# Kernel optimization log

Hardware: AMD Instinct MI355X
Metric: run time of the kernel (lower is better)

Reference implementation:

```python
import jax, jax.numpy as jnp
import numpy as np

N_HEAD = 16
N_KV = 4
HEAD_DIM = 128
ROPE_BASE = 10000.0
YARN_ORIG = 2048
YARN_TARGET = 8192
YARN_ALPHA = 1.0
YARN_BETA = 1.0
SOFTCAP = 50.0


def _yarn_freqs(seq_len, start=0):
    # inv_freq with YaRN scaling: stretch by (target/orig)**alpha, magnitude 1/beta
    inv_freq = 1.0 / (ROPE_BASE ** (jnp.arange(0, HEAD_DIM, 2, dtype=jnp.float32) / HEAD_DIM))
    scale = (YARN_TARGET / YARN_ORIG) ** YARN_ALPHA
    inv_freq = inv_freq / scale * (1.0 / max(YARN_BETA, 1e-6))
    pos = jnp.arange(start, start + seq_len, dtype=jnp.float32)
    return pos[:, None] * inv_freq[None, :]  # [T, D/2]


def _apply_rope(x, freqs):
    # x: [B, H, T, D], interleaved even/odd rotation
    x_even = x[..., ::2]
    x_odd = x[..., 1::2]
    cos = jnp.cos(freqs)[None, None]  # [1,1,T,D/2]
    sin = jnp.sin(freqs)[None, None]
    y_even = x_even * cos - x_odd * sin
    y_odd = x_odd * cos + x_even * sin
    y = jnp.stack([y_even, y_odd], axis=-1).reshape(x.shape)
    return y


def setup_inputs() -> dict:
    key = jax.random.key(0)
    k1, k2, k3 = jax.random.split(key, 3)
    B, T, C = 2, 2048, 2048
    qkv_dim = (N_HEAD + 2 * N_KV) * HEAD_DIM  # 3072
    x = jax.random.normal(k1, (B, T, C), dtype=jnp.float32)
    w_qkv = jax.random.normal(k2, (C, qkv_dim), dtype=jnp.float32) * (1.0 / np.sqrt(C))
    w_o = jax.random.normal(k3, (C, C), dtype=jnp.float32) * (1.0 / np.sqrt(C))
    return {"x": x, "w_qkv": w_qkv, "w_o": w_o}


def reference(x, w_qkv, w_o):
    B, T, C = x.shape
    qkv = x @ w_qkv  # [B, T, (H+2*Hkv)*D]
    q_dim = N_HEAD * HEAD_DIM
    kv_dim = N_KV * HEAD_DIM
    q = qkv[..., :q_dim].reshape(B, T, N_HEAD, HEAD_DIM).transpose(0, 2, 1, 3)
    k = qkv[..., q_dim:q_dim + kv_dim].reshape(B, T, N_KV, HEAD_DIM).transpose(0, 2, 1, 3)
    v = qkv[..., q_dim + kv_dim:].reshape(B, T, N_KV, HEAD_DIM).transpose(0, 2, 1, 3)

    freqs = _yarn_freqs(T)
    q = _apply_rope(q, freqs)
    k = _apply_rope(k, freqs)

    # GQA: expand kv heads to query heads
    rep = N_HEAD // N_KV
    k = jnp.repeat(k, rep, axis=1)
    v = jnp.repeat(v, rep, axis=1)

    scores = jnp.einsum('bhqd,bhkd->bhqk', q, k) / jnp.sqrt(jnp.float32(HEAD_DIM))
    scores = SOFTCAP * jnp.tanh(scores / SOFTCAP)
    causal = jnp.tril(jnp.ones((T, T), dtype=bool))
    scores = jnp.where(causal[None, None], scores, jnp.float32(-1e9))
    attn = jax.nn.softmax(scores.astype(jnp.float32), axis=-1).astype(q.dtype)
    out = jnp.einsum('bhqk,bhkd->bhqd', attn, v)
    out = out.transpose(0, 2, 1, 3).reshape(B, T, C)
    return out @ w_o
```

## Files before the change

kernel.cpp:

```cpp
#include <hip/hip_runtime.h>
#include <hip/hip_bf16.h>

typedef __attribute__((ext_vector_type(8))) __bf16 bf16x8;
typedef __attribute__((ext_vector_type(2))) __bf16 bf16x2;
typedef __attribute__((ext_vector_type(4))) float f32x4;

#define T_SEQ 2048
#define C_DIM 2048
#define QKV_DIM 3072
#define NKV 4
#define HD 128

#define AS1 __attribute__((address_space(1)))
#define AS3 __attribute__((address_space(3)))

__device__ __forceinline__ unsigned short f2bf(float x) {
    __hip_bfloat16 h = __float2bfloat16(x);
    return __builtin_bit_cast(unsigned short, h);
}
__device__ __forceinline__ float bf2f(unsigned short u) {
    unsigned int i = ((unsigned int)u) << 16;
    return __builtin_bit_cast(float, i);
}
__device__ __forceinline__ unsigned int pkbf(float lo, float hi) {
#if __has_builtin(__builtin_amdgcn_cvt_pk_bf16_f32)
    bf16x2 r = __builtin_amdgcn_cvt_pk_bf16_f32(lo, hi);
    return __builtin_bit_cast(unsigned int, r);
#else
    return ((unsigned int)f2bf(hi) << 16) | (unsigned int)f2bf(lo);
#endif
}
__device__ __forceinline__ f32x4 mfma16(bf16x8 a, bf16x8 b, f32x4 c) {
    return __builtin_amdgcn_mfma_f32_16x16x32_bf16(a, b, c, 0, 0, 0);
}
__device__ __forceinline__ void gload_lds16(const void* g, void* l) {
    __builtin_amdgcn_global_load_lds((const AS1 unsigned int*)g,
                                     (AS3 unsigned int*)l, 16, 0, 0);
}
__device__ __forceinline__ float softcap_exp(float s) {
    const float CX2 = 3.125e-6f;
    const float CT  = 0.12752334197529714f;
    float x2 = s * s * CX2;
    float poly = fmaf(x2, fmaf(x2, 0.13333333f, -0.33333333f), 1.0f);
    return exp2f(s * CT * poly);
}

__global__ __launch_bounds__(256) void prep_kernel(
        const float* __restrict__ x, unsigned short* __restrict__ xbf,
        const float* __restrict__ w_qkv, unsigned short* __restrict__ wqkvT,
        const float* __restrict__ w_o, unsigned short* __restrict__ woT,
        float2* __restrict__ tab) {
    __shared__ float tile[32][33];
    int idx = blockIdx.x, tid = threadIdx.x;
    if (idx < 8192) {
        int i = idx * 256 + tid;
        float4 v = ((const float4*)x)[i];
        uint2 o;
        o.x = pkbf(v.x, v.y);
        o.y = pkbf(v.z, v.w);
        ((uint2*)xbf)[i] = o;
        return;
    }
    if (idx < 18432) {
        const float* in;  unsigned short* out;  int rows, cols, bx, by;
        if (idx < 14336) {
            int pid = idx - 8192;
            in = w_qkv; out = wqkvT; rows = 2048; cols = 3072;
            bx = pid % 96; by = pid / 96;
        } else {
            int pid = idx - 14336;
            in = w_o; out = woT; rows = 2048; cols = 2048;
            bx = pid % 64; by = pid / 64;
        }
        int c0 = bx * 32, r0 = by * 32;
        int tx = tid & 31, ty = tid >> 5;
        #pragma unroll
        for (int i = 0; i < 4; i++)
            tile[ty + 8 * i][tx] = in[(size_t)(r0 + ty + 8 * i) * cols + c0 + tx];
        __syncthreads();
        #pragma unroll
        for (int i = 0; i < 4; i++)
            out[(size_t)(c0 + ty + 8 * i) * rows + r0 + tx] = f2bf(tile[tx][ty + 8 * i]);
        return;
    }
    {
        int i2 = (idx - 18432) * 256 + tid;
        int t = i2 >> 6, i = i2 & 63;
        float inv = 0.25f * exp2f(-(float)i * (13.287712379549449f / 64.0f));
        float ang = (float)t * inv;
        float s, c;
        __sincosf(ang, &s, &c);
        tab[i2] = make_float2(c, s);
    }
}

__global__ __launch_bounds__(256) void rope_packv_kernel(
        unsigned short* __restrict__ qkv, const float2* __restrict__ tab,
        unsigned short* __restrict__ kpack, unsigned short* __restrict__ vpack) {
    __shared__ unsigned short stile[32][33];
    int idx = blockIdx.x, tid = threadIdx.x;
    if (idx < 4096) {
        int row = idx;
        int t = row & (T_SEQ - 1);
        int b = row >> 11;
        const float2* tb = tab + t * 64;
        for (int p = tid; p < 1280; p += 256) {
            int head = p >> 6, i = p & 63;
            float2 cs = tb[i];
            size_t qidx = (size_t)row * QKV_DIM + head * 128 + 2 * i;
            unsigned int u = *(const unsigned int*)(qkv + qidx);
            float e = bf2f((unsigned short)(u & 0xffff));
            float o = bf2f((unsigned short)(u >> 16));
            unsigned int res = pkbf(e * cs.x - o * cs.y, o * cs.x + e * cs.y);
            if (head < 16) {
                *(unsigned int*)(qkv + qidx) = res;
            } else {
                int kvh = head - 16;
                unsigned short* dst = kpack +
                    (size_t)((b * NKV + kvh) * 128 + (t >> 4)) * 2048 +
                    (i >> 2) * 128 + (t & 15) * 8 + (i & 3) * 2;
                *(unsigned int*)dst = res;
            }
        }
        return;
    }
    {
        int pid = idx - 4096;
        int c0 = (pid & 15) * 32;
        int r0 = (pid >> 4) * 32;
        int tx = tid & 31, ty = tid >> 5;
        #pragma unroll
        for (int i = 0; i < 4; i++)
            stile[ty + 8 * i][tx] =
                qkv[(size_t)(r0 + ty + 8 * i) * QKV_DIM + 2560 + c0 + tx];
        __syncthreads();
        #pragma unroll
        for (int i = 0; i < 4; i++) {
            int dcol = c0 + ty + 8 * i;
            int kv = dcol >> 7, d = dcol & 127;
            int r = r0 + tx;
            int b = r >> 11, t = r & (T_SEQ - 1);
            vpack[(size_t)((b * NKV + kv) * 64 + (t >> 5)) * 4096 +
                  (d >> 4) * 512 + ((t >> 3) & 3) * 128 + (d & 15) * 8 + (t & 7)] =
                stile[tx][ty + 8 * i];
        }
    }
}

template <int OUT_BF16>
__global__ __launch_bounds__(256) void gemm_bt(
        const unsigned short* __restrict__ A, const unsigned short* __restrict__ Bt,
        void* __restrict__ Cout, int M, int N, int K) {
    __shared__ __align__(16) unsigned short As[128 * 64];
    __shared__ __align__(16) unsigned short Bs[128 * 64];
    int tid = threadIdx.x;
    int nwg = gridDim.x * gridDim.y;
    int lid = blockIdx.y * gridDim.x + blockIdx.x;
    int work = (lid & 7) * (nwg >> 3) + (lid >> 3);
    int m0 = (work % gridDim.y) * 128;
    int n0 = (work / gridDim.y) * 128;
    int wave = tid >> 6, lane = tid & 63;
    int wm = (wave & 1) * 64, wn = (wave >> 1) * 64;
    int l15 = lane & 15, quad = lane >> 4;
    int lrow8 = lane >> 3;
    int swz8 = (lane & 7) ^ lrow8;

    f32x4 zf = {0.f, 0.f, 0.f, 0.f};
    f32x4 acc[4][4];
    #pragma unroll
    for (int i = 0; i < 4; i++)
        #pragma unroll
        for (int j = 0; j < 4; j++) acc[i][j] = zf;

    const unsigned short* gA = A + (size_t)(m0 + wave * 32 + lrow8) * K + swz8 * 8;
    const unsigned short* gB = Bt + (size_t)(n0 + wave * 32 + lrow8) * K + swz8 * 8;
    unsigned short* lA = &As[(wave * 4) * 512];
    unsigned short* lB = &Bs[(wave * 4) * 512];
    int rsw = (l15 & 7) << 3;

    for (int k0 = 0; k0 < K; k0 += 64) {
        #pragma unroll
        for (int l = 0; l < 4; l++) {
            gload_lds16(gA + k0 + (size_t)l * 8 * K, lA + l * 512);
            gload_lds16(gB + k0 + (size_t)l * 8 * K, lB + l * 512);
        }
        __syncthreads();
        #pragma unroll
        for (int kk = 0; kk < 2; kk++) {
            bf16x8 af[4], bfr[4];
            #pragma unroll
            for (int i = 0; i < 4; i++)
                af[i] = *(const bf16x8*)&As[(wm + i * 16 + l15) * 64 +
                                            (((kk * 4 + quad) << 3) ^ rsw)];
            #pragma unroll
            for (int i = 0; i < 4; i++)
                bfr[i] = *(const bf16x8*)&Bs[(wn + i * 16 + l15) * 64 +
                                             (((kk * 4 + quad) << 3) ^ rsw)];
            #pragma unroll
            for (int mi = 0; mi < 4; mi++)
                #pragma unroll
                for (int ni = 0; ni < 4; ni++)
                    acc[mi][ni] = mfma16(af[mi], bfr[ni], acc[mi][ni]);
        }
        __syncthreads();
    }
    #pragma unroll
    for (int mi = 0; mi < 4; mi++)
        #pragma unroll
        for (int ni = 0; ni < 4; ni++) {
            int row = m0 + wm + mi * 16 + quad * 4;
            int col = n0 + wn + ni * 16 + l15;
            #pragma unroll
            for (int r = 0; r < 4; r++) {
                float v = acc[mi][ni][r];
                if (OUT_BF16)
                    ((unsigned short*)Cout)[(size_t)(row + r) * N + col] = f2bf(v);
                else
                    ((float*)Cout)[(size_t)(row + r) * N + col] = v;
            }
        }
}

__device__ __forceinline__ void attn_tile(
        const unsigned short* __restrict__ qkv,
        const unsigned short* __restrict__ kpack,
        const unsigned short* __restrict__ vpack,
        unsigned short* __restrict__ attn_out,
        unsigned int* __restrict__ pT, float* __restrict__ comb,
        int b, int hA, int qt, int wave, int lane) {
    int l15 = lane & 15, quad = lane >> 4;
    int kv = hA >> 2;
    f32x4 zf = {0.f, 0.f, 0.f, 0.f};

    const unsigned short* kb_ = kpack + ((size_t)(b * NKV + kv) * 128) * 2048 + lane * 8;
    const unsigned short* vb_ = vpack + ((size_t)(b * NKV + kv) * 64) * 4096 + lane * 8;

    int n = (qt >> 1) + 1;
    int half = n >> 1;
    int lo = wave ? half : 0;
    int hi = wave ? n : half;

    const unsigned short* qp =
        qkv + (size_t)(b * T_SEQ + qt * 16 + l15) * QKV_DIM + hA * HD + quad * 8;
    bf16x8 aqA[4], aqB[4];
    #pragma unroll
    for (int c = 0; c < 4; c++) {
        aqA[c] = *(const bf16x8*)(qp + c * 32);
        aqB[c] = *(const bf16x8*)(qp + HD + c * 32);
    }

    f32x4 oA[8], oB[8];
    #pragma unroll
    for (int d = 0; d < 8; d++) { oA[d] = zf; oB[d] = zf; }
    float lsA = 0.f, lsB = 0.f;
    int qglob = qt * 16 + l15;

    if (lo < hi) {
        bf16x8 KA[8], KB[8];
        auto loadK = [&](bf16x8* K, int t) {
            const unsigned short* a = kb_ + (size_t)t * 4096;
            #pragma unroll
            for (int c = 0; c < 4; c++) {
                K[c]     = *(const bf16x8*)(a + c * 512);
                K[4 + c] = *(const bf16x8*)(a + 2048 + c * 512);
            }
        };
        auto step = [&](const bf16x8* K, unsigned int* buf, int t,
                        bf16x8* Kpre, bool do_pre) {
            const unsigned short* v0 = vb_ + (size_t)t * 4096;
            bf16x8 Vv[8];
            #pragma unroll
            for (int dd = 0; dd < 8; dd++)
                Vv[dd] = *(const bf16x8*)(v0 + dd * 512);
            if (do_pre) loadK(Kpre, t + 1);
            f32x4 s0A = zf, s1A = zf, s0B = zf, s1B = zf;
            __builtin_amdgcn_s_setprio(1);
            #pragma unroll
            for (int c = 0; c < 4; c++) {
                s0A = mfma16(K[c],     aqA[c], s0A);
                s1A = mfma16(K[4 + c], aqA[c], s1A);
                s0B = mfma16(K[c],     aqB[c], s0B);
                s1B = mfma16(K[4 + c], aqB[c], s1B);
            }
            __builtin_amdgcn_s_setprio(0);
            bool masked = (t == n - 1);
            float p0A[4], p1A[4], p0B[4], p1B[4];
            int kb = t * 32 + quad * 4;
            #pragma unroll
            for (int r = 0; r < 4; r++) {
                float q0A = softcap_exp(s0A[r]);
                float q1A = softcap_exp(s1A[r]);
                float q0B = softcap_exp(s0B[r]);
                float q1B = softcap_exp(s1B[r]);
                if (masked) {
                    bool m0 = (kb + r <= qglob), m1 = (kb + 16 + r <= qglob);
                    q0A = m0 ? q0A : 0.f;  q1A = m1 ? q1A : 0.f;
                    q0B = m0 ? q0B : 0.f;  q1B = m1 ? q1B : 0.f;
                }
                p0A[r] = q0A; p1A[r] = q1A; lsA += q0A + q1A;
                p0B[r] = q0B; p1B[r] = q1B; lsB += q0B + q1B;
            }
            unsigned int* wpA = buf + l15 * 20 + quad * 2;
            unsigned int* wpB = wpA + 320;
            *(uint2*)wpA       = make_uint2(pkbf(p0A[0], p0A[1]), pkbf(p0A[2], p0A[3]));
            *(uint2*)(wpA + 8) = make_uint2(pkbf(p1A[0], p1A[1]), pkbf(p1A[2], p1A[3]));
            *(uint2*)wpB       = make_uint2(pkbf(p0B[0], p0B[1]), pkbf(p0B[2], p0B[3]));
            *(uint2*)(wpB + 8) = make_uint2(pkbf(p1B[0], p1B[1]), pkbf(p1B[2], p1B[3]));
            __asm__ volatile("s_waitcnt lgkmcnt(0)" ::: "memory");
            bf16x8 bpA = *(const bf16x8*)(buf + l15 * 20 + quad * 4);
            bf16x8 bpB = *(const bf16x8*)(buf + 320 + l15 * 20 + quad * 4);
            __builtin_amdgcn_s_setprio(1);
            #pragma unroll
            for (int dd = 0; dd < 8; dd++) {
                oA[dd] = mfma16(Vv[dd], bpA, oA[dd]);
                oB[dd] = mfma16(Vv[dd], bpB, oB[dd]);
            }
            __builtin_amdgcn_s_setprio(0);
        };

        loadK(KA, lo);
        int t = lo;
        while (true) {
            bool last = (t == hi - 1);
            step(KA, pT, t, KB, !last);
            if (last) break;
            t++;
            last = (t == hi - 1);
            step(KB, pT + 640, t, KA, !last);
            if (last) break;
            t++;
        }
    }

    float* slot = comb + lane * 34;
    if (wave == 0) {
        #pragma unroll
        for (int dd = 0; dd < 8; dd++)
            #pragma unroll
            for (int r = 0; r < 4; r++) slot[dd * 4 + r] = oB[dd][r];
        slot[32] = lsB;
    }
    __syncthreads();
    if (wave == 1) {
        #pragma unroll
        for (int dd = 0; dd < 8; dd++)
            #pragma unroll
            for (int r = 0; r < 4; r++) oB[dd][r] += slot[dd * 4 + r];
        lsB += slot[32];
        float l = lsB;
        l += __shfl_xor(l, 16);
        l += __shfl_xor(l, 32);
        float rl = __builtin_amdgcn_rcpf(l);
        unsigned short* op = attn_out +
            (size_t)(b * T_SEQ + qt * 16 + l15) * C_DIM + (hA + 1) * HD + quad * 4;
        #pragma unroll
        for (int dd = 0; dd < 8; dd++) {
            unsigned int u0 = pkbf(oB[dd][0] * rl, oB[dd][1] * rl);
            unsigned int u1 = pkbf(oB[dd][2] * rl, oB[dd][3] * rl);
            *(uint2*)(op + dd * 16) = make_uint2(u0, u1);
        }
    }
    __syncthreads();
    if (wave == 1) {
        #pragma unroll
        for (int dd = 0; dd < 8; dd++)
            #pragma unroll
            for (int r = 0; r < 4; r++) slot[dd * 4 + r] = oA[dd][r];
        slot[32] = lsA;
    }
    __syncthreads();
    if (wave == 0) {
        #pragma unroll
        for (int dd = 0; dd < 8; dd++)
            #pragma unroll
            for (int r = 0; r < 4; r++) oA[dd][r] += slot[dd * 4 + r];
        lsA += slot[32];
        float l = lsA;
        l += __shfl_xor(l, 16);
        l += __shfl_xor(l, 32);
        float rl = __builtin_amdgcn_rcpf(l);
        unsigned short* op = attn_out +
            (size_t)(b * T_SEQ + qt * 16 + l15) * C_DIM + hA * HD + quad * 4;
        #pragma unroll
        for (int dd = 0; dd < 8; dd++) {
            unsigned int u0 = pkbf(oA[dd][0] * rl, oA[dd][1] * rl);
            unsigned int u1 = pkbf(oA[dd][2] * rl, oA[dd][3] * rl);
            *(uint2*)(op + dd * 16) = make_uint2(u0, u1);
        }
    }
}

__global__ __launch_bounds__(128) void attn_kernel(
        const unsigned short* __restrict__ qkv,
        const unsigned short* __restrict__ kpack,
        const unsigned short* __restrict__ vpack,
        unsigned short* __restrict__ attn_out) {
    __shared__ __align__(16) unsigned int pT[2][1280];
    __shared__ float comb[64 * 34];
    int bid = blockIdx.x;
    int qt = 127 - (bid >> 4);
    int g = bid & 15;
    int b = g >> 3, pair = g & 7;
    int hA = pair * 2;
    int wave = threadIdx.x >> 6, lane = threadIdx.x & 63;
    attn_tile(qkv, kpack, vpack, attn_out, pT[wave], comb, b, hA, qt, wave, lane);
}

extern "C" void kernel_launch(void* const* d_in, const int* in_sizes, int n_in,
                              void* d_out, int out_size, void* d_ws, size_t ws_size,
                              hipStream_t stream) {
    (void)in_sizes; (void)n_in; (void)out_size; (void)ws_size;
    const float* x = (const float*)d_in[0];
    const float* w_qkv = (const float*)d_in[1];
    const float* w_o = (const float*)d_in[2];
    char* ws = (char*)d_ws;

    unsigned short* xbf   = (unsigned short*)(ws);
    unsigned short* wqkvT = (unsigned short*)(ws + 16777216);
    unsigned short* woT   = (unsigned short*)(ws + 29360128);
    unsigned short* qkv   = (unsigned short*)(ws + 37748736);
    unsigned short* kpack = (unsigned short*)(ws + 16777216);
    unsigned short* vpack = (unsigned short*)(ws + 20971520);
    float2*         tab   = (float2*)(ws + 62914560);
    unsigned short* attn  = xbf;

    prep_kernel<<<18944, 256, 0, stream>>>(x, xbf, w_qkv, wqkvT, w_o, woT, tab);
    gemm_bt<1><<<dim3(24, 32), 256, 0, stream>>>(xbf, wqkvT, qkv, 4096, 3072, 2048);
    rope_packv_kernel<<<6144, 256, 0, stream>>>(qkv, tab, kpack, vpack);
    attn_kernel<<<2048, 128, 0, stream>>>(qkv, kpack, vpack, attn);
    gemm_bt<0><<<dim3(16, 32), 256, 0, stream>>>(attn, woT, d_out, 4096, 2048, 2048);
}
```

Baseline: 329.5 us.

## Split attention KV range across four waves and pair causal q-tiles per block

```diff
diff --git a/kernel.cpp b/kernel.cpp
--- a/kernel.cpp
+++ b/kernel.cpp
@@ -221,13 +221,13 @@
         }
 }
 
-__device__ __forceinline__ void attn_tile(
+__device__ __forceinline__ void attn_tile4(
         const unsigned short* __restrict__ qkv,
         const unsigned short* __restrict__ kpack,
         const unsigned short* __restrict__ vpack,
         unsigned short* __restrict__ attn_out,
         unsigned int* __restrict__ pT, float* __restrict__ comb,
-        int b, int hA, int qt, int wave, int lane) {
+        int b, int hA, int j, int wave, int lane) {
     int l15 = lane & 15, quad = lane >> 4;
     int kv = hA >> 2;
     f32x4 zf = {0.f, 0.f, 0.f, 0.f};
@@ -235,175 +235,188 @@
     const unsigned short* kb_ = kpack + ((size_t)(b * NKV + kv) * 128) * 2048 + lane * 8;
     const unsigned short* vb_ = vpack + ((size_t)(b * NKV + kv) * 64) * 4096 + lane * 8;
 
-    int n = (qt >> 1) + 1;
-    int half = n >> 1;
-    int lo = wave ? half : 0;
-    int hi = wave ? n : half;
-
-    const unsigned short* qp =
-        qkv + (size_t)(b * T_SEQ + qt * 16 + l15) * QKV_DIM + hA * HD + quad * 8;
-    bf16x8 aqA[4], aqB[4];
-    #pragma unroll
-    for (int c = 0; c < 4; c++) {
-        aqA[c] = *(const bf16x8*)(qp + c * 32);
-        aqB[c] = *(const bf16x8*)(qp + HD + c * 32);
-    }
-
-    f32x4 oA[8], oB[8];
-    #pragma unroll
-    for (int d = 0; d < 8; d++) { oA[d] = zf; oB[d] = zf; }
-    float lsA = 0.f, lsB = 0.f;
-    int qglob = qt * 16 + l15;
-
-    if (lo < hi) {
-        bf16x8 KA[8], KB[8];
-        auto loadK = [&](bf16x8* K, int t) {
-            const unsigned short* a = kb_ + (size_t)t * 4096;
-            #pragma unroll
-            for (int c = 0; c < 4; c++) {
-                K[c]     = *(const bf16x8*)(a + c * 512);
-                K[4 + c] = *(const bf16x8*)(a + 2048 + c * 512);
-            }
-        };
-        auto step = [&](const bf16x8* K, unsigned int* buf, int t,
-                        bf16x8* Kpre, bool do_pre) {
-            const unsigned short* v0 = vb_ + (size_t)t * 4096;
-            bf16x8 Vv[8];
+    for (int pass = 0; pass < 2; pass++) {
+        int qt = pass ? (127 - j) : j;
+        int n = (qt >> 1) + 1;
+        int lo = (n * wave) >> 2;
+        int hi = (n * (wave + 1)) >> 2;
+
+        const unsigned short* qp =
+            qkv + (size_t)(b * T_SEQ + qt * 16 + l15) * QKV_DIM + hA * HD + quad * 8;
+        bf16x8 aqA[4], aqB[4];
+        #pragma unroll
+        for (int c = 0; c < 4; c++) {
+            aqA[c] = *(const bf16x8*)(qp + c * 32);
+            aqB[c] = *(const bf16x8*)(qp + HD + c * 32);
+        }
+
+        f32x4 oA[8], oB[8];
+        #pragma unroll
+        for (int d = 0; d < 8; d++) { oA[d] = zf; oB[d] = zf; }
+        float lsA = 0.f, lsB = 0.f;
+        int qglob = qt * 16 + l15;
+
+        if (lo < hi) {
+            bf16x8 KA[8], KB[8];
+            auto loadK = [&](bf16x8* K, int t) {
+                const unsigned short* a = kb_ + (size_t)t * 4096;
+                #pragma unroll
+                for (int c = 0; c < 4; c++) {
+                    K[c]     = *(const bf16x8*)(a + c * 512);
+                    K[4 + c] = *(const bf16x8*)(a + 2048 + c * 512);
+                }
+            };
+            auto step = [&](const bf16x8* K, unsigned int* buf, int t,
+                            bf16x8* Kpre, bool do_pre) {
+                const unsigned short* v0 = vb_ + (size_t)t * 4096;
+                bf16x8 Vv[8];
+                #pragma unroll
+                for (int dd = 0; dd < 8; dd++)
+                    Vv[dd] = *(const bf16x8*)(v0 + dd * 512);
+                if (do_pre) loadK(Kpre, t + 1);
+                f32x4 s0A = zf, s1A = zf, s0B = zf, s1B = zf;
+                __builtin_amdgcn_s_setprio(1);
+                #pragma unroll
+                for (int c = 0; c < 4; c++) {
+                    s0A = mfma16(K[c],     aqA[c], s0A);
+                    s1A = mfma16(K[4 + c], aqA[c], s1A);
+                    s0B = mfma16(K[c],     aqB[c], s0B);
+                    s1B = mfma16(K[4 + c], aqB[c], s1B);
+                }
+                __builtin_amdgcn_s_setprio(0);
+                bool masked = (t == n - 1);
+                float p0A[4], p1A[4], p0B[4], p1B[4];
+                int kb = t * 32 + quad * 4;
+                #pragma unroll
+                for (int r = 0; r < 4; r++) {
+                    float q0A = softcap_exp(s0A[r]);
+                    float q1A = softcap_exp(s1A[r]);
+                    float q0B = softcap_exp(s0B[r]);
+                    float q1B = softcap_exp(s1B[r]);
+                    if (masked) {
+                        bool m0 = (kb + r <= qglob), m1 = (kb + 16 + r <= qglob);
+                        q0A = m0 ? q0A : 0.f;  q1A = m1 ? q1A : 0.f;
+                        q0B = m0 ? q0B : 0.f;  q1B = m1 ? q1B : 0.f;
+                    }
+                    p0A[r] = q0A; p1A[r] = q1A; lsA += q0A + q1A;
+                    p0B[r] = q0B; p1B[r] = q1B; lsB += q0B + q1B;
+                }
+                unsigned int* wpA = buf + l15 * 20 + quad * 2;
+                unsigned int* wpB = wpA + 320;
+                *(uint2*)wpA       = make_uint2(pkbf(p0A[0], p0A[1]), pkbf(p0A[2], p0A[3]));
+                *(uint2*)(wpA + 8) = make_uint2(pkbf(p1A[0], p1A[1]), pkbf(p1A[2], p1A[3]));
+                *(uint2*)wpB       = make_uint2(pkbf(p0B[0], p0B[1]), pkbf(p0B[2], p0B[3]));
+                *(uint2*)(wpB + 8) = make_uint2(pkbf(p1B[0], p1B[1]), pkbf(p1B[2], p1B[3]));
+                __asm__ volatile("s_waitcnt lgkmcnt(0)" ::: "memory");
+                bf16x8 bpA = *(const bf16x8*)(buf + l15 * 20 + quad * 4);
+                bf16x8 bpB = *(const bf16x8*)(buf + 320 + l15 * 20 + quad * 4);
+                __builtin_amdgcn_s_setprio(1);
+                #pragma unroll
+                for (int dd = 0; dd < 8; dd++) {
+                    oA[dd] = mfma16(Vv[dd], bpA, oA[dd]);
+                    oB[dd] = mfma16(Vv[dd], bpB, oB[dd]);
+                }
+                __builtin_amdgcn_s_setprio(0);
+            };
+
+            loadK(KA, lo);
+            int t = lo;
+            while (true) {
+                bool last = (t == hi - 1);
+                step(KA, pT, t, KB, !last);
+                if (last) break;
+                t++;
+                last = (t == hi - 1);
+                step(KB, pT + 640, t, KA, !last);
+                if (last) break;
+                t++;
+            }
+        }
+
+        if (wave >= 1) {
+            float* s = comb + (wave - 1) * 2112 + lane * 33;
             #pragma unroll
             for (int dd = 0; dd < 8; dd++)
-                Vv[dd] = *(const bf16x8*)(v0 + dd * 512);
-            if (do_pre) loadK(Kpre, t + 1);
-            f32x4 s0A = zf, s1A = zf, s0B = zf, s1B = zf;
-            __builtin_amdgcn_s_setprio(1);
-            #pragma unroll
-            for (int c = 0; c < 4; c++) {
-                s0A = mfma16(K[c],     aqA[c], s0A);
-                s1A = mfma16(K[4 + c], aqA[c], s1A);
-                s0B = mfma16(K[c],     aqB[c], s0B);
-                s1B = mfma16(K[4 + c], aqB[c], s1B);
-            }
-            __builtin_amdgcn_s_setprio(0);
-            bool masked = (t == n - 1);
-            float p0A[4], p1A[4], p0B[4], p1B[4];
-            int kb = t * 32 + quad * 4;
-            #pragma unroll
-            for (int r = 0; r < 4; r++) {
-                float q0A = softcap_exp(s0A[r]);
-                float q1A = softcap_exp(s1A[r]);
-                float q0B = softcap_exp(s0B[r]);
-                float q1B = softcap_exp(s1B[r]);
-                if (masked) {
-                    bool m0 = (kb + r <= qglob), m1 = (kb + 16 + r <= qglob);
-                    q0A = m0 ? q0A : 0.f;  q1A = m1 ? q1A : 0.f;
-                    q0B = m0 ? q0B : 0.f;  q1B = m1 ? q1B : 0.f;
-                }
-                p0A[r] = q0A; p1A[r] = q1A; lsA += q0A + q1A;
-                p0B[r] = q0B; p1B[r] = q1B; lsB += q0B + q1B;
-            }
-            unsigned int* wpA = buf + l15 * 20 + quad * 2;
-            unsigned int* wpB = wpA + 320;
-            *(uint2*)wpA       = make_uint2(pkbf(p0A[0], p0A[1]), pkbf(p0A[2], p0A[3]));
-            *(uint2*)(wpA + 8) = make_uint2(pkbf(p1A[0], p1A[1]), pkbf(p1A[2], p1A[3]));
-            *(uint2*)wpB       = make_uint2(pkbf(p0B[0], p0B[1]), pkbf(p0B[2], p0B[3]));
-            *(uint2*)(wpB + 8) = make_uint2(pkbf(p1B[0], p1B[1]), pkbf(p1B[2], p1B[3]));
-            __asm__ volatile("s_waitcnt lgkmcnt(0)" ::: "memory");
-            bf16x8 bpA = *(const bf16x8*)(buf + l15 * 20 + quad * 4);
-            bf16x8 bpB = *(const bf16x8*)(buf + 320 + l15 * 20 + quad * 4);
-            __builtin_amdgcn_s_setprio(1);
+                #pragma unroll
+                for (int r = 0; r < 4; r++) s[dd * 4 + r] = oA[dd][r];
+            s[32] = lsA;
+        }
+        __syncthreads();
+        if (wave == 0) {
+            #pragma unroll
+            for (int k = 0; k < 3; k++) {
+                float* s = comb + k * 2112 + lane * 33;
+                #pragma unroll
+                for (int dd = 0; dd < 8; dd++)
+                    #pragma unroll
+                    for (int r = 0; r < 4; r++) oA[dd][r] += s[dd * 4 + r];
+                lsA += s[32];
+            }
+            float l = lsA;
+            l += __shfl_xor(l, 16);
+            l += __shfl_xor(l, 32);
+            float rl = __builtin_amdgcn_rcpf(l);
+            unsigned short* op = attn_out +
+                (size_t)(b * T_SEQ + qt * 16 + l15) * C_DIM + hA * HD + quad * 4;
             #pragma unroll
             for (int dd = 0; dd < 8; dd++) {
-                oA[dd] = mfma16(Vv[dd], bpA, oA[dd]);
-                oB[dd] = mfma16(Vv[dd], bpB, oB[dd]);
-            }
-            __builtin_amdgcn_s_setprio(0);
-        };
-
-        loadK(KA, lo);
-        int t = lo;
-        while (true) {
-            bool last = (t == hi - 1);
-            step(KA, pT, t, KB, !last);
-            if (last) break;
-            t++;
-            last = (t == hi - 1);
-            step(KB, pT + 640, t, KA, !last);
-            if (last) break;
-            t++;
-        }
-    }
-
-    float* slot = comb + lane * 34;
-    if (wave == 0) {
-        #pragma unroll
-        for (int dd = 0; dd < 8; dd++)
-            #pragma unroll
-            for (int r = 0; r < 4; r++) slot[dd * 4 + r] = oB[dd][r];
-        slot[32] = lsB;
-    }
-    __syncthreads();
-    if (wave == 1) {
-        #pragma unroll
-        for (int dd = 0; dd < 8; dd++)
-            #pragma unroll
-            for (int r = 0; r < 4; r++) oB[dd][r] += slot[dd * 4 + r];
-        lsB += slot[32];
-        float l = lsB;
-        l += __shfl_xor(l, 16);
-        l += __shfl_xor(l, 32);
-        float rl = __builtin_amdgcn_rcpf(l);
-        unsigned short* op = attn_out +
-            (size_t)(b * T_SEQ + qt * 16 + l15) * C_DIM + (hA + 1) * HD + quad * 4;
-        #pragma unroll
-        for (int dd = 0; dd < 8; dd++) {
-            unsigned int u0 = pkbf(oB[dd][0] * rl, oB[dd][1] * rl);
-            unsigned int u1 = pkbf(oB[dd][2] * rl, oB[dd][3] * rl);
-            *(uint2*)(op + dd * 16) = make_uint2(u0, u1);
-        }
-    }
-    __syncthreads();
-    if (wave == 1) {
-        #pragma unroll
-        for (int dd = 0; dd < 8; dd++)
-            #pragma unroll
-            for (int r = 0; r < 4; r++) slot[dd * 4 + r] = oA[dd][r];
-        slot[32] = lsA;
-    }
-    __syncthreads();
-    if (wave == 0) {
-        #pragma unroll
-        for (int dd = 0; dd < 8; dd++)
-            #pragma unroll
-            for (int r = 0; r < 4; r++) oA[dd][r] += slot[dd * 4 + r];
-        lsA += slot[32];
-        float l = lsA;
-        l += __shfl_xor(l, 16);
-        l += __shfl_xor(l, 32);
-        float rl = __builtin_amdgcn_rcpf(l);
-        unsigned short* op = attn_out +
-            (size_t)(b * T_SEQ + qt * 16 + l15) * C_DIM + hA * HD + quad * 4;
-        #pragma unroll
-        for (int dd = 0; dd < 8; dd++) {
-            unsigned int u0 = pkbf(oA[dd][0] * rl, oA[dd][1] * rl);
-            unsigned int u1 = pkbf(oA[dd][2] * rl, oA[dd][3] * rl);
-            *(uint2*)(op + dd * 16) = make_uint2(u0, u1);
-        }
-    }
-}
-
-__global__ __launch_bounds__(128) void attn_kernel(
+                unsigned int u0 = pkbf(oA[dd][0] * rl, oA[dd][1] * rl);
+                unsigned int u1 = pkbf(oA[dd][2] * rl, oA[dd][3] * rl);
+                *(uint2*)(op + dd * 16) = make_uint2(u0, u1);
+            }
+        }
+        __syncthreads();
+        if (wave != 1) {
+            int s3 = (wave == 0) ? 0 : (wave - 1);
+            float* s = comb + s3 * 2112 + lane * 33;
+            #pragma unroll
+            for (int dd = 0; dd < 8; dd++)
+                #pragma unroll
+                for (int r = 0; r < 4; r++) s[dd * 4 + r] = oB[dd][r];
+            s[32] = lsB;
+        }
+        __syncthreads();
+        if (wave == 1) {
+            #pragma unroll
+            for (int k = 0; k < 3; k++) {
+                float* s = comb + k * 2112 + lane * 33;
+                #pragma unroll
+                for (int dd = 0; dd < 8; dd++)
+                    #pragma unroll
+                    for (int r = 0; r < 4; r++) oB[dd][r] += s[dd * 4 + r];
+                lsB += s[32];
+            }
+            float l = lsB;
+            l += __shfl_xor(l, 16);
+            l += __shfl_xor(l, 32);
+            float rl = __builtin_amdgcn_rcpf(l);
+            unsigned short* op = attn_out +
+                (size_t)(b * T_SEQ + qt * 16 + l15) * C_DIM + (hA + 1) * HD + quad * 4;
+            #pragma unroll
+            for (int dd = 0; dd < 8; dd++) {
+                unsigned int u0 = pkbf(oB[dd][0] * rl, oB[dd][1] * rl);
+                unsigned int u1 = pkbf(oB[dd][2] * rl, oB[dd][3] * rl);
+                *(uint2*)(op + dd * 16) = make_uint2(u0, u1);
+            }
+        }
+        __syncthreads();
+    }
+}
+
+__global__ __launch_bounds__(256) void attn_kernel(
         const unsigned short* __restrict__ qkv,
         const unsigned short* __restrict__ kpack,
         const unsigned short* __restrict__ vpack,
         unsigned short* __restrict__ attn_out) {
-    __shared__ __align__(16) unsigned int pT[2][1280];
-    __shared__ float comb[64 * 34];
+    __shared__ __align__(16) unsigned int pT[4][1280];
+    __shared__ float comb[3 * 2112];
     int bid = blockIdx.x;
-    int qt = 127 - (bid >> 4);
+    int j = bid >> 4;
     int g = bid & 15;
     int b = g >> 3, pair = g & 7;
     int hA = pair * 2;
     int wave = threadIdx.x >> 6, lane = threadIdx.x & 63;
-    attn_tile(qkv, kpack, vpack, attn_out, pT[wave], comb, b, hA, qt, wave, lane);
+    attn_tile4(qkv, kpack, vpack, attn_out, pT[wave], comb, b, hA, j, wave, lane);
 }
 
 extern "C" void kernel_launch(void* const* d_in, const int* in_sizes, int n_in,
@@ -427,6 +440,6 @@
     prep_kernel<<<18944, 256, 0, stream>>>(x, xbf, w_qkv, wqkvT, w_o, woT, tab);
     gemm_bt<1><<<dim3(24, 32), 256, 0, stream>>>(xbf, wqkvT, qkv, 4096, 3072, 2048);
     rope_packv_kernel<<<6144, 256, 0, stream>>>(qkv, tab, kpack, vpack);
-    attn_kernel<<<2048, 128, 0, stream>>>(qkv, kpack, vpack, attn);
+    attn_kernel<<<1024, 256, 0, stream>>>(qkv, kpack, vpack, attn);
     gemm_bt<0><<<dim3(16, 32), 256, 0, stream>>>(attn, woT, d_out, 4096, 2048, 2048);
 }
```

After: 341.9 us. 3.8% more time.

## Software-pipeline QK^T one tile ahead of softmax and PV

Applied to the files above, without the earlier changes.

```diff
diff --git a/kernel.cpp b/kernel.cpp
--- a/kernel.cpp
+++ b/kernel.cpp
@@ -265,33 +265,36 @@
                 K[4 + c] = *(const bf16x8*)(a + 2048 + c * 512);
             }
         };
-        auto step = [&](const bf16x8* K, unsigned int* buf, int t,
-                        bf16x8* Kpre, bool do_pre) {
+        auto qkcalc = [&](const bf16x8* K, f32x4* s) {
+            s[0] = zf; s[1] = zf; s[2] = zf; s[3] = zf;
+            __builtin_amdgcn_s_setprio(1);
+            #pragma unroll
+            for (int c = 0; c < 4; c++) {
+                s[0] = mfma16(K[c],     aqA[c], s[0]);
+                s[1] = mfma16(K[4 + c], aqA[c], s[1]);
+                s[2] = mfma16(K[c],     aqB[c], s[2]);
+                s[3] = mfma16(K[4 + c], aqB[c], s[3]);
+            }
+            __builtin_amdgcn_s_setprio(0);
+        };
+        auto step = [&](unsigned int* buf, int t, bf16x8* Kfree,
+                        const bf16x8* Knext, f32x4* sc, f32x4* sn) {
+            bool lastT = (t == hi - 1);
             const unsigned short* v0 = vb_ + (size_t)t * 4096;
             bf16x8 Vv[8];
             #pragma unroll
             for (int dd = 0; dd < 8; dd++)
                 Vv[dd] = *(const bf16x8*)(v0 + dd * 512);
-            if (do_pre) loadK(Kpre, t + 1);
-            f32x4 s0A = zf, s1A = zf, s0B = zf, s1B = zf;
-            __builtin_amdgcn_s_setprio(1);
-            #pragma unroll
-            for (int c = 0; c < 4; c++) {
-                s0A = mfma16(K[c],     aqA[c], s0A);
-                s1A = mfma16(K[4 + c], aqA[c], s1A);
-                s0B = mfma16(K[c],     aqB[c], s0B);
-                s1B = mfma16(K[4 + c], aqB[c], s1B);
-            }
-            __builtin_amdgcn_s_setprio(0);
+            if (t + 2 < hi) loadK(Kfree, t + 2);
             bool masked = (t == n - 1);
             float p0A[4], p1A[4], p0B[4], p1B[4];
             int kb = t * 32 + quad * 4;
             #pragma unroll
             for (int r = 0; r < 4; r++) {
-                float q0A = softcap_exp(s0A[r]);
-                float q1A = softcap_exp(s1A[r]);
-                float q0B = softcap_exp(s0B[r]);
-                float q1B = softcap_exp(s1B[r]);
+                float q0A = softcap_exp(sc[0][r]);
+                float q1A = softcap_exp(sc[1][r]);
+                float q0B = softcap_exp(sc[2][r]);
+                float q1B = softcap_exp(sc[3][r]);
                 if (masked) {
                     bool m0 = (kb + r <= qglob), m1 = (kb + 16 + r <= qglob);
                     q0A = m0 ? q0A : 0.f;  q1A = m1 ? q1A : 0.f;
@@ -306,6 +309,7 @@
             *(uint2*)(wpA + 8) = make_uint2(pkbf(p1A[0], p1A[1]), pkbf(p1A[2], p1A[3]));
             *(uint2*)wpB       = make_uint2(pkbf(p0B[0], p0B[1]), pkbf(p0B[2], p0B[3]));
             *(uint2*)(wpB + 8) = make_uint2(pkbf(p1B[0], p1B[1]), pkbf(p1B[2], p1B[3]));
+            if (!lastT) qkcalc(Knext, sn);
             __asm__ volatile("s_waitcnt lgkmcnt(0)" ::: "memory");
             bf16x8 bpA = *(const bf16x8*)(buf + l15 * 20 + quad * 4);
             bf16x8 bpB = *(const bf16x8*)(buf + 320 + l15 * 20 + quad * 4);
@@ -318,16 +322,17 @@
             __builtin_amdgcn_s_setprio(0);
         };
 
+        f32x4 sc[4], sn[4];
         loadK(KA, lo);
+        if (lo + 1 < hi) loadK(KB, lo + 1);
+        qkcalc(KA, sc);
         int t = lo;
         while (true) {
-            bool last = (t == hi - 1);
-            step(KA, pT, t, KB, !last);
-            if (last) break;
+            step(pT, t, KA, KB, sc, sn);
+            if (t == hi - 1) break;
             t++;
-            last = (t == hi - 1);
-            step(KB, pT + 640, t, KA, !last);
-            if (last) break;
+            step(pT + 640, t, KB, KA, sn, sc);
+            if (t == hi - 1) break;
             t++;
         }
     }
```

Result: faster. 317.2 us (-3.7%).
